# Optimization experiments

Hardware: AMD Instinct MI355X
Metric: run time of the kernel (lower is better)

Reference implementation:

```python
import jax, jax.numpy as jnp
import numpy as np

B, T, C = 2, 2048, 1024
H = 16
HD = C // H  # 64


def setup_inputs() -> dict:
    key = jax.random.key(0)
    ks = jax.random.split(key, 6)
    s_in = 1.0 / np.sqrt(C)
    s_pr = 1.0 / np.sqrt(H * HD)
    x = jax.random.normal(ks[0], (B, T, C), dtype=jnp.float32)
    Wq = jax.random.uniform(ks[1], (H, C, HD), jnp.float32, -s_in, s_in)
    Wk = jax.random.uniform(ks[2], (H, C, HD), jnp.float32, -s_in, s_in)
    Wv = jax.random.uniform(ks[3], (H, C, HD), jnp.float32, -s_in, s_in)
    Wp = jax.random.uniform(ks[4], (H * HD, C), jnp.float32, -s_pr, s_pr)
    bp = jax.random.uniform(ks[5], (C,), jnp.float32, -s_pr, s_pr)
    return {"x": x, "Wq": Wq, "Wk": Wk, "Wv": Wv, "Wp": Wp, "bp": bp}


def reference(x, Wq, Wk, Wv, Wp, bp):
    # per-head projections: [B,T,C] x [H,C,D] -> [B,H,T,D]
    q = jnp.einsum('btc,hcd->bhtd', x, Wq)
    k = jnp.einsum('btc,hcd->bhtd', x, Wk)
    v = jnp.einsum('btc,hcd->bhtd', x, Wv)
    scale = HD ** (-0.5)
    scores = jnp.einsum('bhtd,bhsd->bhts', q, k) * scale  # [B,H,T,T]
    causal = jnp.tril(jnp.ones((T, T), dtype=bool))
    scores = jnp.where(causal, scores, -jnp.inf)
    w = jax.nn.softmax(scores, axis=-1)
    out = jnp.einsum('bhts,bhsd->bhtd', w, v)  # [B,H,T,D]
    # concat heads: [B,T,H*D] (head order matches torch.cat over heads)
    out = jnp.transpose(out, (0, 2, 1, 3)).reshape(B, T, H * HD)
    return out @ Wp + bp
```

## Files before the change

### kernel.cpp

```cpp
#include <hip/hip_runtime.h>
#include <hip/hip_bf16.h>

#define B_NUM 2
#define T_SEQ 2048
#define C_DIM 1024
#define H_NUM 16
#define HD    64
#define M_TOT 4096
#define BH_N  32

typedef __attribute__((ext_vector_type(8))) short short8;
typedef __attribute__((ext_vector_type(4))) float floatx4;

__device__ __forceinline__ short f2bf(float f) {
    unsigned u = __float_as_uint(f);
    u += 0x7FFFu + ((u >> 16) & 1u);
    return (short)(u >> 16);
}

__device__ __forceinline__ unsigned pk2bf(float a, float b) {
    float2 f2; f2.x = a; f2.y = b;
    __hip_bfloat162 h = __float22bfloat162_rn(f2);
    unsigned u; __builtin_memcpy(&u, &h, 4); return u;
}

__device__ __forceinline__ void gld16(const short* g, short* l) {
    __builtin_amdgcn_global_load_lds(
        (const __attribute__((address_space(1))) void*)g,
        (__attribute__((address_space(3))) void*)l, 16, 0, 0);
}

__global__ __launch_bounds__(256) void prep(
    const float* __restrict__ x, const float* __restrict__ Wq,
    const float* __restrict__ Wk, const float* __restrict__ Wv,
    const float* __restrict__ Wp,
    short* __restrict__ xb, short* __restrict__ wt, short* __restrict__ wpt) {
    const int bid = blockIdx.x;
    const int tid = threadIdx.x;
    if (bid < 2048) {
        int idx = (bid * 256 + tid) * 8;
        float4 a = *(const float4*)(x + idx);
        float4 b = *(const float4*)(x + idx + 4);
        short8 o;
        o[0] = f2bf(a.x); o[1] = f2bf(a.y); o[2] = f2bf(a.z); o[3] = f2bf(a.w);
        o[4] = f2bf(b.x); o[5] = f2bf(b.y); o[6] = f2bf(b.z); o[7] = f2bf(b.w);
        *(short8*)(xb + idx) = o;
        return;
    }
    const int b2 = bid - 2048;
    const int ct = b2 & 15, y = b2 >> 4;
    __shared__ short sh[64][72];
    if (y < 48) {
        const int which = y >> 4, h = y & 15;
        const float* W = ((which == 0) ? Wq : (which == 1) ? Wk : Wv) + (size_t)h * C_DIM * HD;
        const int c0 = ct * 64;
        #pragma unroll
        for (int p = 0; p < 4; ++p) {
            int idx = tid + 256 * p;
            int c = idx >> 4, d4 = idx & 15;
            float4 v = *(const float4*)(W + (size_t)(c0 + c) * HD + d4 * 4);
            sh[d4 * 4 + 0][c] = f2bf(v.x);
            sh[d4 * 4 + 1][c] = f2bf(v.y);
            sh[d4 * 4 + 2][c] = f2bf(v.z);
            sh[d4 * 4 + 3][c] = f2bf(v.w);
        }
        __syncthreads();
        #pragma unroll
        for (int p = 0; p < 2; ++p) {
            int idx = tid + 256 * p;
            int d = idx >> 3, cc = idx & 7;
            short8 vv = *(const short8*)(&sh[d][cc * 8]);
            *(short8*)(wt + ((size_t)(which * 16 + h) * 64 + d) * C_DIM + c0 + cc * 8) = vv;
        }
    } else {
        const int nt = y - 48;
        #pragma unroll
        for (int p = 0; p < 4; ++p) {
            int idx = tid + 256 * p;
            int k = idx >> 4, n4 = idx & 15;
            float4 v = *(const float4*)(Wp + (size_t)(ct * 64 + k) * C_DIM + nt * 64 + n4 * 4);
            sh[n4 * 4 + 0][k] = f2bf(v.x);
            sh[n4 * 4 + 1][k] = f2bf(v.y);
            sh[n4 * 4 + 2][k] = f2bf(v.z);
            sh[n4 * 4 + 3][k] = f2bf(v.w);
        }
        __syncthreads();
        #pragma unroll
        for (int p = 0; p < 2; ++p) {
            int idx = tid + 256 * p;
            int n = idx >> 3, cc = idx & 7;
            short8 vv = *(const short8*)(&sh[n][cc * 8]);
            *(short8*)(wpt + (size_t)(nt * 64 + n) * C_DIM + ct * 64 + cc * 8) = vv;
        }
    }
}

__global__ __launch_bounds__(256) void qkv_gemm(
    const short* __restrict__ xb, const short* __restrict__ wt,
    short* __restrict__ qb, short* __restrict__ kb, short* __restrict__ vtb) {
    const int mt = blockIdx.x, ntg = blockIdx.y;
    const int m0 = mt * 128, n0 = ntg * 128;
    const int which = ntg >> 3;
    const float sc = (which == 0) ? 0.125f * 1.4426950408889634f : 1.0f;

    __shared__ short smem[17408];
    short* As = smem;
    short* Bs = smem + 8192;

    const int tid = threadIdx.x;
    const int lane = tid & 63, w = tid >> 6;
    const int wm = w & 1, wn = w >> 1;
    const int hi = lane >> 4, llo = lane & 15;
    const int lrow = lane >> 3;
    const int lswz = ((lane & 7) ^ (lrow & 7)) * 8;
    const int fc0 = (hi ^ (llo & 7)) * 8;
    const int fc1 = ((hi + 4) ^ (llo & 7)) * 8;

    floatx4 acc[4][4];
    #pragma unroll
    for (int i = 0; i < 4; ++i)
        #pragma unroll
        for (int j = 0; j < 4; ++j)
            #pragma unroll
            for (int r = 0; r < 4; ++r) acc[i][j][r] = 0.0f;

    const size_t a_base = (size_t)(m0 + w * 32 + lrow) * C_DIM + lswz;
    const size_t b_base = (size_t)(n0 + w * 32 + lrow) * C_DIM + lswz;

    for (int kt = 0; kt < C_DIM / 64; ++kt) {
        const int c0 = kt * 64;
        __syncthreads();
        #pragma unroll
        for (int p = 0; p < 4; ++p) {
            gld16(xb + a_base + (size_t)p * 8 * C_DIM + c0, &As[(w * 32 + p * 8) * 64]);
            gld16(wt + b_base + (size_t)p * 8 * C_DIM + c0, &Bs[(w * 32 + p * 8) * 64]);
        }
        __syncthreads();

        short8 af[4][2];
        #pragma unroll
        for (int mi = 0; mi < 4; ++mi) {
            const int row = wm * 64 + mi * 16 + llo;
            af[mi][0] = *(const short8*)(&As[row * 64 + fc0]);
            af[mi][1] = *(const short8*)(&As[row * 64 + fc1]);
        }
        #pragma unroll
        for (int ni = 0; ni < 4; ++ni) {
            const int row = wn * 64 + ni * 16 + llo;
            short8 b0 = *(const short8*)(&Bs[row * 64 + fc0]);
            short8 b1 = *(const short8*)(&Bs[row * 64 + fc1]);
            #pragma unroll
            for (int mi = 0; mi < 4; ++mi) {
                acc[mi][ni] = __builtin_amdgcn_mfma_f32_16x16x32_bf16(af[mi][0], b0, acc[mi][ni], 0, 0, 0);
                acc[mi][ni] = __builtin_amdgcn_mfma_f32_16x16x32_bf16(af[mi][1], b1, acc[mi][ni], 0, 0, 0);
            }
        }
    }
    __syncthreads();

    short (*R)[136] = (short(*)[136])smem;
    if (which == 2) {
        #pragma unroll
        for (int mi = 0; mi < 4; ++mi)
            #pragma unroll
            for (int ni = 0; ni < 4; ++ni)
                #pragma unroll
                for (int r = 0; r < 4; ++r)
                    R[wn * 64 + ni * 16 + llo][wm * 64 + mi * 16 + hi * 4 + r] =
                        f2bf(acc[mi][ni][r]);
        __syncthreads();
        const int b = m0 >> 11;
        #pragma unroll
        for (int p = 0; p < 8; ++p) {
            int idx = tid + 256 * p;
            int rr = idx >> 4, cc = idx & 15;
            short8 vv = *(const short8*)(&R[rr][cc * 8]);
            int n = n0 + rr;
            int h = (n >> 6) & 15, d = n & 63;
            int t = (m0 & 2047) + cc * 8;
            *(short8*)(vtb + ((size_t)((b * H_NUM + h) * HD + d)) * T_SEQ + t) = vv;
        }
    } else {
        short* outp = (which == 0) ? qb : kb;
        #pragma unroll
        for (int mi = 0; mi < 4; ++mi)
            #pragma unroll
            for (int ni = 0; ni < 4; ++ni)
                #pragma unroll
                for (int r = 0; r < 4; ++r)
                    R[wm * 64 + mi * 16 + hi * 4 + r][wn * 64 + ni * 16 + llo] =
                        f2bf(acc[mi][ni][r] * sc);
        __syncthreads();
        #pragma unroll
        for (int p = 0; p < 8; ++p) {
            int idx = tid + 256 * p;
            int r = idx >> 4, cc = idx & 15;
            short8 vv = *(const short8*)(&R[r][cc * 8]);
            int mg = m0 + r;
            int b = mg >> 11, t = mg & 2047;
            int n = n0 + cc * 8;
            int h = (n >> 6) & 15, d = n & 63;
            *(short8*)(outp + ((size_t)(b * H_NUM + h) * T_SEQ + t) * HD + d) = vv;
        }
    }
}

__global__ __launch_bounds__(512) void attn_mfma(
    const short* __restrict__ qb, const short* __restrict__ kb,
    const short* __restrict__ vtb, short* __restrict__ attb) {
    const int bh = blockIdx.x;
    const int y = blockIdx.y;
    const int qt = (y < 8) ? (15 - y) : (y - 8);
    const int b = bh >> 4, h = bh & 15;
    const short* K  = kb  + (size_t)bh * T_SEQ * HD;
    const short* Vt = vtb + (size_t)bh * HD * T_SEQ;

    __shared__ short Ks[2][4096];
    __shared__ short Vs[2][4096];
    __shared__ short Ones[16 * 64];
    __shared__ short Ps[128][76];

    const int tid = threadIdx.x;
    const int lane = tid & 63, w = tid >> 6;
    const int hi = lane >> 4, llo = lane & 15;
    const int lrow = lane >> 3;
    const int lswz = ((lane & 7) ^ (lrow & 7)) * 8;
    const int fc0 = (hi ^ (llo & 7)) * 8;
    const int fc1 = ((hi + 4) ^ (llo & 7)) * 8;
    const int kmax = 2 * qt + 1;

    short8 qf[2];
    const int qcol0 = qt * 128 + w * 16;
    #pragma unroll
    for (int kh = 0; kh < 2; ++kh)
        qf[kh] = *(const short8*)(qb +
            ((size_t)bh * T_SEQ + qcol0 + llo) * HD + kh * 32 + hi * 8);

    for (int i = tid; i < 16 * 64; i += 512)
        Ones[i] = (i < 64) ? (short)0x3F80 : (short)0;

    gld16(K + (size_t)(w * 8 + lrow) * HD + lswz, &Ks[0][(w * 8) * 64]);
    gld16(Vt + (size_t)(w * 8 + lrow) * T_SEQ + lswz, &Vs[0][(w * 8) * 64]);

    floatx4 Oa[5];
    #pragma unroll
    for (int n = 0; n < 5; ++n)
        #pragma unroll
        for (int r = 0; r < 4; ++r) Oa[n][r] = 0.0f;

    for (int kt = 0; kt <= kmax; ++kt) {
        __syncthreads();
        const int buf = kt & 1;

        if (kt + 1 <= kmax) {
            const int s0 = (kt + 1) * 64;
            const int nb = buf ^ 1;
            gld16(K + ((size_t)s0 + w * 8 + lrow) * HD + lswz, &Ks[nb][(w * 8) * 64]);
            gld16(Vt + (size_t)(w * 8 + lrow) * T_SEQ + s0 + lswz, &Vs[nb][(w * 8) * 64]);
        }

        short8 ak[4][2];
        #pragma unroll
        for (int nt = 0; nt < 4; ++nt) {
            const int row = nt * 16 + llo;
            ak[nt][0] = *(const short8*)(&Ks[buf][row * 64 + fc0]);
            ak[nt][1] = *(const short8*)(&Ks[buf][row * 64 + fc1]);
        }
        floatx4 sf[4];
        #pragma unroll
        for (int nt = 0; nt < 4; ++nt)
            #pragma unroll
            for (int r = 0; r < 4; ++r) sf[nt][r] = 0.0f;
        #pragma unroll
        for (int nt = 0; nt < 4; ++nt)
            #pragma unroll
            for (int kh = 0; kh < 2; ++kh)
                sf[nt] = __builtin_amdgcn_mfma_f32_16x16x32_bf16(
                    ak[nt][kh], qf[kh], sf[nt], 0, 0, 0);

        const int sbase = kt * 64;
        if (sbase + 63 > qcol0) {
            const int qlane = qcol0 + llo;
            #pragma unroll
            for (int nt = 0; nt < 4; ++nt)
                #pragma unroll
                for (int r = 0; r < 4; ++r)
                    if (sbase + nt * 16 + hi * 4 + r > qlane) sf[nt][r] = -3.0e38f;
        }

        #pragma unroll
        for (int nt = 0; nt < 4; ++nt) {
            float p0 = __builtin_amdgcn_exp2f(sf[nt][0]);
            float p1 = __builtin_amdgcn_exp2f(sf[nt][1]);
            float p2 = __builtin_amdgcn_exp2f(sf[nt][2]);
            float p3 = __builtin_amdgcn_exp2f(sf[nt][3]);
            uint2 u; u.x = pk2bf(p0, p1); u.y = pk2bf(p2, p3);
            *(uint2*)(&Ps[w * 16 + llo][nt * 16 + hi * 4]) = u;
        }

        short8 av[5][2];
        #pragma unroll
        for (int nt2 = 0; nt2 < 4; ++nt2) {
            const int row = nt2 * 16 + llo;
            av[nt2][0] = *(const short8*)(&Vs[buf][row * 64 + fc0]);
            av[nt2][1] = *(const short8*)(&Vs[buf][row * 64 + fc1]);
        }
        av[4][0] = *(const short8*)(&Ones[llo * 64 + fc0]);
        av[4][1] = *(const short8*)(&Ones[llo * 64 + fc1]);
        short8 bp[2];
        #pragma unroll
        for (int kh = 0; kh < 2; ++kh)
            bp[kh] = *(const short8*)(&Ps[w * 16 + llo][kh * 32 + hi * 8]);
        #pragma unroll
        for (int nt2 = 0; nt2 < 5; ++nt2)
            #pragma unroll
            for (int kh = 0; kh < 2; ++kh)
                Oa[nt2] = __builtin_amdgcn_mfma_f32_16x16x32_bf16(
                    av[nt2][kh], bp[kh], Oa[nt2], 0, 0, 0);
    }

    {
        float lb = __shfl(Oa[4][0], llo);
        float inv = 1.0f / lb;
        #pragma unroll
        for (int nt2 = 0; nt2 < 4; ++nt2) {
            uint2 u;
            u.x = pk2bf(Oa[nt2][0] * inv, Oa[nt2][1] * inv);
            u.y = pk2bf(Oa[nt2][2] * inv, Oa[nt2][3] * inv);
            *(uint2*)(&Ps[w * 16 + llo][nt2 * 16 + hi * 4]) = u;
        }
    }
    __syncthreads();
    #pragma unroll
    for (int p = 0; p < 2; ++p) {
        int idx = tid + 512 * p;
        int r = idx >> 3, cc = idx & 7;
        short8 vv = *(const short8*)(&Ps[r][cc * 8]);
        *(short8*)(attb + ((size_t)(b * T_SEQ + qt * 128 + r)) * C_DIM + h * HD + cc * 8) = vv;
    }
}

__global__ __launch_bounds__(256) void proj_gemm(
    const short* __restrict__ attb, const short* __restrict__ wpt,
    const float* __restrict__ bp, float* __restrict__ out) {
    const int mt = blockIdx.x, nt_g = blockIdx.y;
    const int m0 = mt * 128, n0 = nt_g * 64;

    __shared__ short As[8192];
    __shared__ short Bs[4096];

    const int tid = threadIdx.x;
    const int lane = tid & 63, w = tid >> 6;
    const int hi = lane >> 4, llo = lane & 15;
    const int lrow = lane >> 3;
    const int lswz = ((lane & 7) ^ (lrow & 7)) * 8;
    const int fc0 = (hi ^ (llo & 7)) * 8;
    const int fc1 = ((hi + 4) ^ (llo & 7)) * 8;

    floatx4 acc[2][4];
    #pragma unroll
    for (int i = 0; i < 2; ++i)
        #pragma unroll
        for (int j = 0; j < 4; ++j)
            #pragma unroll
            for (int r = 0; r < 4; ++r) acc[i][j][r] = 0.0f;

    const size_t a_base = (size_t)(m0 + w * 32 + lrow) * C_DIM + lswz;
    const size_t b_base = (size_t)(n0 + w * 16 + lrow) * C_DIM + lswz;

    for (int kt = 0; kt < C_DIM / 64; ++kt) {
        const int c0 = kt * 64;
        __syncthreads();
        #pragma unroll
        for (int p = 0; p < 4; ++p)
            gld16(attb + a_base + (size_t)p * 8 * C_DIM + c0, &As[(w * 32 + p * 8) * 64]);
        #pragma unroll
        for (int p = 0; p < 2; ++p)
            gld16(wpt + b_base + (size_t)p * 8 * C_DIM + c0, &Bs[(w * 16 + p * 8) * 64]);
        __syncthreads();

        short8 af[2][2];
        #pragma unroll
        for (int m2 = 0; m2 < 2; ++m2) {
            const int row = w * 32 + m2 * 16 + llo;
            af[m2][0] = *(const short8*)(&As[row * 64 + fc0]);
            af[m2][1] = *(const short8*)(&As[row * 64 + fc1]);
        }
        #pragma unroll
        for (int nt = 0; nt < 4; ++nt) {
            const int row = nt * 16 + llo;
            short8 b0 = *(const short8*)(&Bs[row * 64 + fc0]);
            short8 b1 = *(const short8*)(&Bs[row * 64 + fc1]);
            #pragma unroll
            for (int m2 = 0; m2 < 2; ++m2) {
                acc[m2][nt] = __builtin_amdgcn_mfma_f32_16x16x32_bf16(af[m2][0], b0, acc[m2][nt], 0, 0, 0);
                acc[m2][nt] = __builtin_amdgcn_mfma_f32_16x16x32_bf16(af[m2][1], b1, acc[m2][nt], 0, 0, 0);
            }
        }
    }

    #pragma unroll
    for (int nt = 0; nt < 4; ++nt) {
        const int n = n0 + nt * 16 + llo;
        const float bias = bp[n];
        #pragma unroll
        for (int m2 = 0; m2 < 2; ++m2)
            #pragma unroll
            for (int r = 0; r < 4; ++r) {
                int m = m0 + w * 32 + m2 * 16 + hi * 4 + r;
                out[(size_t)m * C_DIM + n] = acc[m2][nt][r] + bias;
            }
    }
}

extern "C" void kernel_launch(void* const* d_in, const int* in_sizes, int n_in,
                              void* d_out, int out_size, void* d_ws, size_t ws_size,
                              hipStream_t stream) {
    const float* x  = (const float*)d_in[0];
    const float* Wq = (const float*)d_in[1];
    const float* Wk = (const float*)d_in[2];
    const float* Wv = (const float*)d_in[3];
    const float* Wp = (const float*)d_in[4];
    const float* bp = (const float*)d_in[5];
    float* out = (float*)d_out;

    short* xb   = (short*)d_ws;
    short* wt   = xb  + (size_t)M_TOT * C_DIM;
    short* wpt  = wt  + (size_t)3 * H_NUM * HD * C_DIM;
    short* qb   = wpt + (size_t)C_DIM * C_DIM;
    short* kb   = qb  + (size_t)M_TOT * C_DIM;
    short* vtb  = kb  + (size_t)M_TOT * C_DIM;
    short* attb = vtb + (size_t)M_TOT * C_DIM;

    prep     <<<dim3(3072), 256, 0, stream>>>(x, Wq, Wk, Wv, Wp, xb, wt, wpt);
    qkv_gemm <<<dim3(M_TOT / 128, 3 * C_DIM / 128), 256, 0, stream>>>(xb, wt, qb, kb, vtb);
    attn_mfma<<<dim3(BH_N, T_SEQ / 128), 512, 0, stream>>>(qb, kb, vtb, attb);
    proj_gemm<<<dim3(M_TOT / 128, C_DIM / 64), 256, 0, stream>>>(attb, wpt, bp, out);
}
```

Baseline: 179.4 us.

## Fuse all four stages into one cooperative persistent kernel with grid syncs

Replaces the four separate launches (prep, QKV GEMM, attention, projection) with a single persistent cooperative kernel that loops over work units per stage and separates the stages with grid.sync(). The QKV GEMM tile also changes to 128x192 with 512 threads. The goal is to remove launch gaps and tail effects between kernels. The cost is grid-wide barriers, a fixed grid of 256 or 512 blocks that may load-balance worse than the old grids, and added register and LDS pressure from one shared buffer sized for every stage. The original kernels remain as a fallback if the cooperative launch fails.

```diff
diff --git a/kernel.cpp b/kernel.cpp
--- a/kernel.cpp
+++ b/kernel.cpp
@@ -1,5 +1,8 @@
 #include <hip/hip_runtime.h>
 #include <hip/hip_bf16.h>
+#include <hip/hip_cooperative_groups.h>
+
+namespace cg = cooperative_groups;
 
 #define B_NUM 2
 #define T_SEQ 2048
@@ -30,7 +33,376 @@
         (__attribute__((address_space(3))) void*)l, 16, 0, 0);
 }
 
-__global__ __launch_bounds__(256) void prep(
+__global__ __launch_bounds__(512, 4) void mega(
+    const float* __restrict__ x,  const float* __restrict__ Wq,
+    const float* __restrict__ Wk, const float* __restrict__ Wv,
+    const float* __restrict__ Wp, const float* __restrict__ bp,
+    short* __restrict__ xb, short* __restrict__ wt, short* __restrict__ wpt,
+    short* __restrict__ qb, short* __restrict__ kb, short* __restrict__ vtb,
+    short* __restrict__ attb, float* __restrict__ out) {
+
+    __shared__ short smem[26112];
+    cg::grid_group grid = cg::this_grid();
+
+    const int G   = gridDim.x;
+    const int bid = blockIdx.x;
+    const int tid = threadIdx.x;
+    const int lane = tid & 63, w = tid >> 6;
+    const int hi = lane >> 4, llo = lane & 15;
+    const int lrow = lane >> 3;
+    const int lswz = ((lane & 7) ^ (lrow & 7)) * 8;
+    const int fc0 = (hi ^ (llo & 7)) * 8;
+    const int fc1 = ((hi + 4) ^ (llo & 7)) * 8;
+
+    {
+        int gtid = bid * 512 + tid;
+        for (int i = gtid; i < 524288; i += G * 512) {
+            int idx = i * 8;
+            float4 a = *(const float4*)(x + idx);
+            float4 b4 = *(const float4*)(x + idx + 4);
+            short8 o;
+            o[0] = f2bf(a.x);  o[1] = f2bf(a.y);  o[2] = f2bf(a.z);  o[3] = f2bf(a.w);
+            o[4] = f2bf(b4.x); o[5] = f2bf(b4.y); o[6] = f2bf(b4.z); o[7] = f2bf(b4.w);
+            *(short8*)(xb + idx) = o;
+        }
+        short (*sh)[72] = (short(*)[72])smem;
+        for (int unit = bid; unit < 1024; unit += G) {
+            __syncthreads();
+            if (unit < 768) {
+                const int y = unit >> 4, ct = unit & 15;
+                const int which = y >> 4, h = y & 15;
+                const float* W = ((which == 0) ? Wq : (which == 1) ? Wk : Wv)
+                                 + (size_t)h * C_DIM * HD;
+                const int c0 = ct * 64;
+                #pragma unroll
+                for (int p = 0; p < 2; ++p) {
+                    int idx = tid + 512 * p;
+                    int c = idx >> 4, d4 = idx & 15;
+                    float4 v = *(const float4*)(W + (size_t)(c0 + c) * HD + d4 * 4);
+                    sh[d4 * 4 + 0][c] = f2bf(v.x);
+                    sh[d4 * 4 + 1][c] = f2bf(v.y);
+                    sh[d4 * 4 + 2][c] = f2bf(v.z);
+                    sh[d4 * 4 + 3][c] = f2bf(v.w);
+                }
+                __syncthreads();
+                int d = tid >> 3, cc = tid & 7;
+                short8 vv = *(const short8*)(&sh[d][cc * 8]);
+                *(short8*)(wt + ((size_t)(which * 16 + h) * 64 + d) * C_DIM + c0 + cc * 8) = vv;
+            } else {
+                const int u2 = unit - 768;
+                const int nt = u2 >> 4, ct = u2 & 15;
+                #pragma unroll
+                for (int p = 0; p < 2; ++p) {
+                    int idx = tid + 512 * p;
+                    int k = idx >> 4, n4 = idx & 15;
+                    float4 v = *(const float4*)(Wp + (size_t)(ct * 64 + k) * C_DIM + nt * 64 + n4 * 4);
+                    sh[n4 * 4 + 0][k] = f2bf(v.x);
+                    sh[n4 * 4 + 1][k] = f2bf(v.y);
+                    sh[n4 * 4 + 2][k] = f2bf(v.z);
+                    sh[n4 * 4 + 3][k] = f2bf(v.w);
+                }
+                __syncthreads();
+                int n = tid >> 3, cc = tid & 7;
+                short8 vv = *(const short8*)(&sh[n][cc * 8]);
+                *(short8*)(wpt + (size_t)(nt * 64 + n) * C_DIM + ct * 64 + cc * 8) = vv;
+            }
+        }
+    }
+    grid.sync();
+
+    for (int tile = bid; tile < 512; tile += G) {
+        const int mt = tile >> 4, ntg = tile & 15;
+        const int m0 = mt * 128, n0 = ntg * 192;
+        const int wm = w & 1, wn = w >> 1;
+        short* As = smem;
+        short* Bs = smem + 8192;
+
+        floatx4 acc[4][3];
+        #pragma unroll
+        for (int i = 0; i < 4; ++i)
+            #pragma unroll
+            for (int j = 0; j < 3; ++j)
+                #pragma unroll
+                for (int r = 0; r < 4; ++r) acc[i][j][r] = 0.0f;
+
+        const size_t a_base = (size_t)(m0 + w * 16 + lrow) * C_DIM + lswz;
+        const size_t b_base = (size_t)(n0 + w * 24 + lrow) * C_DIM + lswz;
+
+        for (int kt = 0; kt < C_DIM / 64; ++kt) {
+            const int c0 = kt * 64;
+            __syncthreads();
+            #pragma unroll
+            for (int p = 0; p < 2; ++p)
+                gld16(xb + a_base + (size_t)p * 8 * C_DIM + c0, &As[(w * 16 + p * 8) * 64]);
+            #pragma unroll
+            for (int p = 0; p < 3; ++p)
+                gld16(wt + b_base + (size_t)p * 8 * C_DIM + c0, &Bs[(w * 24 + p * 8) * 64]);
+            __syncthreads();
+
+            short8 af[4][2];
+            #pragma unroll
+            for (int mi = 0; mi < 4; ++mi) {
+                const int row = wm * 64 + mi * 16 + llo;
+                af[mi][0] = *(const short8*)(&As[row * 64 + fc0]);
+                af[mi][1] = *(const short8*)(&As[row * 64 + fc1]);
+            }
+            #pragma unroll
+            for (int ni = 0; ni < 3; ++ni) {
+                const int row = wn * 48 + ni * 16 + llo;
+                short8 b0 = *(const short8*)(&Bs[row * 64 + fc0]);
+                short8 b1 = *(const short8*)(&Bs[row * 64 + fc1]);
+                #pragma unroll
+                for (int mi = 0; mi < 4; ++mi) {
+                    acc[mi][ni] = __builtin_amdgcn_mfma_f32_16x16x32_bf16(af[mi][0], b0, acc[mi][ni], 0, 0, 0);
+                    acc[mi][ni] = __builtin_amdgcn_mfma_f32_16x16x32_bf16(af[mi][1], b1, acc[mi][ni], 0, 0, 0);
+                }
+            }
+        }
+
+        const int bb = m0 >> 11;
+        #pragma unroll
+        for (int c = 0; c < 3; ++c) {
+            const int n_chunk = n0 + 64 * c;
+            const int which = n_chunk >> 10;
+            const int h = (n_chunk >> 6) & 15;
+            __syncthreads();
+            if (which == 2) {
+                short (*R)[136] = (short(*)[136])smem;
+                #pragma unroll
+                for (int ni = 0; ni < 3; ++ni) {
+                    const int gcol = wn * 48 + ni * 16;
+                    if ((gcol >> 6) == c) {
+                        #pragma unroll
+                        for (int mi = 0; mi < 4; ++mi)
+                            #pragma unroll
+                            for (int r = 0; r < 4; ++r)
+                                R[(gcol & 63) + llo][wm * 64 + mi * 16 + hi * 4 + r] =
+                                    f2bf(acc[mi][ni][r]);
+                    }
+                }
+                __syncthreads();
+                #pragma unroll
+                for (int p = 0; p < 2; ++p) {
+                    int idx = tid + 512 * p;
+                    int rr = idx >> 4, cc = idx & 15;
+                    short8 vv = *(const short8*)(&R[rr][cc * 8]);
+                    int t = (m0 & 2047) + cc * 8;
+                    *(short8*)(vtb + ((size_t)((bb * H_NUM + h) * HD + rr)) * T_SEQ + t) = vv;
+                }
+            } else {
+                short (*R)[72] = (short(*)[72])smem;
+                const float scl = (which == 0) ? 0.125f * 1.4426950408889634f : 1.0f;
+                #pragma unroll
+                for (int ni = 0; ni < 3; ++ni) {
+                    const int gcol = wn * 48 + ni * 16;
+                    if ((gcol >> 6) == c) {
+                        #pragma unroll
+                        for (int mi = 0; mi < 4; ++mi)
+                            #pragma unroll
+                            for (int r = 0; r < 4; ++r)
+                                R[wm * 64 + mi * 16 + hi * 4 + r][(gcol & 63) + llo] =
+                                    f2bf(acc[mi][ni][r] * scl);
+                    }
+                }
+                __syncthreads();
+                short* outp = (which == 0) ? qb : kb;
+                #pragma unroll
+                for (int p = 0; p < 2; ++p) {
+                    int idx = tid + 512 * p;
+                    int r = idx >> 3, cc = idx & 7;
+                    short8 vv = *(const short8*)(&R[r][cc * 8]);
+                    int t = (m0 + r) & 2047;
+                    *(short8*)(outp + ((size_t)(bb * H_NUM + h) * T_SEQ + t) * HD + cc * 8) = vv;
+                }
+            }
+        }
+    }
+    grid.sync();
+
+    for (int unit = bid; unit < 512; unit += G) {
+        const int bh = unit & 31;
+        const int y = unit >> 5;
+        const int qt = (y < 8) ? (15 - y) : (y - 8);
+        const int b = bh >> 4, h = bh & 15;
+        const short* K  = kb  + (size_t)bh * T_SEQ * HD;
+        const short* Vt = vtb + (size_t)bh * HD * T_SEQ;
+
+        short* Ks = smem;
+        short* Vs = smem + 8192;
+        short (*Ps)[76] = (short(*)[76])(smem + 16384);
+
+        const int kmax = 2 * qt + 1;
+
+        short8 qf[2];
+        const int qcol0 = qt * 128 + w * 16;
+        #pragma unroll
+        for (int kh = 0; kh < 2; ++kh)
+            qf[kh] = *(const short8*)(qb +
+                ((size_t)bh * T_SEQ + qcol0 + llo) * HD + kh * 32 + hi * 8);
+
+        short8 av4;
+        #pragma unroll
+        for (int j = 0; j < 8; ++j) av4[j] = (llo == 0) ? (short)0x3F80 : (short)0;
+
+        gld16(K + (size_t)(w * 8 + lrow) * HD + lswz, &Ks[(w * 8) * 64]);
+        gld16(Vt + (size_t)(w * 8 + lrow) * T_SEQ + lswz, &Vs[(w * 8) * 64]);
+
+        floatx4 Oa[5];
+        #pragma unroll
+        for (int n = 0; n < 5; ++n)
+            #pragma unroll
+            for (int r = 0; r < 4; ++r) Oa[n][r] = 0.0f;
+
+        for (int kt = 0; kt <= kmax; ++kt) {
+            __syncthreads();
+            const int buf = (kt & 1) * 4096;
+
+            if (kt + 1 <= kmax) {
+                const int s0 = (kt + 1) * 64;
+                const int nb = ((kt + 1) & 1) * 4096;
+                gld16(K + ((size_t)s0 + w * 8 + lrow) * HD + lswz, &Ks[nb + (w * 8) * 64]);
+                gld16(Vt + (size_t)(w * 8 + lrow) * T_SEQ + s0 + lswz, &Vs[nb + (w * 8) * 64]);
+            }
+
+            short8 ak[4][2];
+            #pragma unroll
+            for (int nt = 0; nt < 4; ++nt) {
+                const int row = nt * 16 + llo;
+                ak[nt][0] = *(const short8*)(&Ks[buf + row * 64 + fc0]);
+                ak[nt][1] = *(const short8*)(&Ks[buf + row * 64 + fc1]);
+            }
+            floatx4 sf[4];
+            #pragma unroll
+            for (int nt = 0; nt < 4; ++nt)
+                #pragma unroll
+                for (int r = 0; r < 4; ++r) sf[nt][r] = 0.0f;
+            #pragma unroll
+            for (int nt = 0; nt < 4; ++nt)
+                #pragma unroll
+                for (int kh = 0; kh < 2; ++kh)
+                    sf[nt] = __builtin_amdgcn_mfma_f32_16x16x32_bf16(
+                        ak[nt][kh], qf[kh], sf[nt], 0, 0, 0);
+
+            const int sbase = kt * 64;
+            if (sbase + 63 > qcol0) {
+                const int qlane = qcol0 + llo;
+                #pragma unroll
+                for (int nt = 0; nt < 4; ++nt)
+                    #pragma unroll
+                    for (int r = 0; r < 4; ++r)
+                        if (sbase + nt * 16 + hi * 4 + r > qlane) sf[nt][r] = -3.0e38f;
+            }
+
+            #pragma unroll
+            for (int nt = 0; nt < 4; ++nt) {
+                float p0 = __builtin_amdgcn_exp2f(sf[nt][0]);
+                float p1 = __builtin_amdgcn_exp2f(sf[nt][1]);
+                float p2 = __builtin_amdgcn_exp2f(sf[nt][2]);
+                float p3 = __builtin_amdgcn_exp2f(sf[nt][3]);
+                uint2 u; u.x = pk2bf(p0, p1); u.y = pk2bf(p2, p3);
+                *(uint2*)(&Ps[w * 16 + llo][nt * 16 + hi * 4]) = u;
+            }
+
+            short8 av[5][2];
+            #pragma unroll
+            for (int nt2 = 0; nt2 < 4; ++nt2) {
+                const int row = nt2 * 16 + llo;
+                av[nt2][0] = *(const short8*)(&Vs[buf + row * 64 + fc0]);
+                av[nt2][1] = *(const short8*)(&Vs[buf + row * 64 + fc1]);
+            }
+            av[4][0] = av4;
+            av[4][1] = av4;
+            short8 bpf[2];
+            #pragma unroll
+            for (int kh = 0; kh < 2; ++kh)
+                bpf[kh] = *(const short8*)(&Ps[w * 16 + llo][kh * 32 + hi * 8]);
+            #pragma unroll
+            for (int nt2 = 0; nt2 < 5; ++nt2)
+                #pragma unroll
+                for (int kh = 0; kh < 2; ++kh)
+                    Oa[nt2] = __builtin_amdgcn_mfma_f32_16x16x32_bf16(
+                        av[nt2][kh], bpf[kh], Oa[nt2], 0, 0, 0);
+        }
+
+        {
+            float lb = __shfl(Oa[4][0], llo);
+            float inv = 1.0f / lb;
+            #pragma unroll
+            for (int nt2 = 0; nt2 < 4; ++nt2) {
+                uint2 u;
+                u.x = pk2bf(Oa[nt2][0] * inv, Oa[nt2][1] * inv);
+                u.y = pk2bf(Oa[nt2][2] * inv, Oa[nt2][3] * inv);
+                *(uint2*)(&Ps[w * 16 + llo][nt2 * 16 + hi * 4]) = u;
+            }
+        }
+        __syncthreads();
+        #pragma unroll
+        for (int p = 0; p < 2; ++p) {
+            int idx = tid + 512 * p;
+            int r = idx >> 3, cc = idx & 7;
+            short8 vv = *(const short8*)(&Ps[r][cc * 8]);
+            *(short8*)(attb + ((size_t)(b * T_SEQ + qt * 128 + r)) * C_DIM + h * HD + cc * 8) = vv;
+        }
+        __syncthreads();
+    }
+    grid.sync();
+
+    for (int tile = bid; tile < 512; tile += G) {
+        const int mt = tile >> 4, ntg = tile & 15;
+        const int m0 = mt * 128, n0 = ntg * 64;
+        const int wm = w & 1, wn = w >> 1;
+        short* As = smem;
+        short* Bs = smem + 8192;
+
+        floatx4 acc[4];
+        #pragma unroll
+        for (int i = 0; i < 4; ++i)
+            #pragma unroll
+            for (int r = 0; r < 4; ++r) acc[i][r] = 0.0f;
+
+        const size_t a_base = (size_t)(m0 + w * 16 + lrow) * C_DIM + lswz;
+        const size_t b_base = (size_t)(n0 + w * 8 + lrow) * C_DIM + lswz;
+
+        for (int kt = 0; kt < C_DIM / 64; ++kt) {
+            const int c0 = kt * 64;
+            __syncthreads();
+            #pragma unroll
+            for (int p = 0; p < 2; ++p)
+                gld16(attb + a_base + (size_t)p * 8 * C_DIM + c0, &As[(w * 16 + p * 8) * 64]);
+            gld16(wpt + b_base + c0, &Bs[(w * 8) * 64]);
+            __syncthreads();
+
+            short8 af[4][2];
+            #pragma unroll
+            for (int mi = 0; mi < 4; ++mi) {
+                const int row = wm * 64 + mi * 16 + llo;
+                af[mi][0] = *(const short8*)(&As[row * 64 + fc0]);
+                af[mi][1] = *(const short8*)(&As[row * 64 + fc1]);
+            }
+            const int brow = wn * 16 + llo;
+            short8 b0 = *(const short8*)(&Bs[brow * 64 + fc0]);
+            short8 b1 = *(const short8*)(&Bs[brow * 64 + fc1]);
+            #pragma unroll
+            for (int mi = 0; mi < 4; ++mi) {
+                acc[mi] = __builtin_amdgcn_mfma_f32_16x16x32_bf16(af[mi][0], b0, acc[mi], 0, 0, 0);
+                acc[mi] = __builtin_amdgcn_mfma_f32_16x16x32_bf16(af[mi][1], b1, acc[mi], 0, 0, 0);
+            }
+        }
+
+        const int n = n0 + wn * 16 + llo;
+        const float bias = bp[n];
+        #pragma unroll
+        for (int mi = 0; mi < 4; ++mi)
+            #pragma unroll
+            for (int r = 0; r < 4; ++r) {
+                int m = m0 + wm * 64 + mi * 16 + hi * 4 + r;
+                out[(size_t)m * C_DIM + n] = acc[mi][r] + bias;
+            }
+        __syncthreads();
+    }
+}
+
+__global__ __launch_bounds__(256) void prep_k(
     const float* __restrict__ x, const float* __restrict__ Wq,
     const float* __restrict__ Wk, const float* __restrict__ Wv,
     const float* __restrict__ Wp,
@@ -95,7 +467,7 @@
     }
 }
 
-__global__ __launch_bounds__(256) void qkv_gemm(
+__global__ __launch_bounds__(256) void qkv_k(
     const short* __restrict__ xb, const short* __restrict__ wt,
     short* __restrict__ qb, short* __restrict__ kb, short* __restrict__ vtb) {
     const int mt = blockIdx.x, ntg = blockIdx.y;
@@ -205,7 +577,7 @@
     }
 }
 
-__global__ __launch_bounds__(512) void attn_mfma(
+__global__ __launch_bounds__(512) void attn_k(
     const short* __restrict__ qb, const short* __restrict__ kb,
     const short* __restrict__ vtb, short* __restrict__ attb) {
     const int bh = blockIdx.x;
@@ -307,16 +679,16 @@
         }
         av[4][0] = *(const short8*)(&Ones[llo * 64 + fc0]);
         av[4][1] = *(const short8*)(&Ones[llo * 64 + fc1]);
-        short8 bp[2];
+        short8 bpf[2];
         #pragma unroll
         for (int kh = 0; kh < 2; ++kh)
-            bp[kh] = *(const short8*)(&Ps[w * 16 + llo][kh * 32 + hi * 8]);
+            bpf[kh] = *(const short8*)(&Ps[w * 16 + llo][kh * 32 + hi * 8]);
         #pragma unroll
         for (int nt2 = 0; nt2 < 5; ++nt2)
             #pragma unroll
             for (int kh = 0; kh < 2; ++kh)
                 Oa[nt2] = __builtin_amdgcn_mfma_f32_16x16x32_bf16(
-                    av[nt2][kh], bp[kh], Oa[nt2], 0, 0, 0);
+                    av[nt2][kh], bpf[kh], Oa[nt2], 0, 0, 0);
     }
 
     {
@@ -340,7 +712,7 @@
     }
 }
 
-__global__ __launch_bounds__(256) void proj_gemm(
+__global__ __launch_bounds__(256) void proj_k(
     const short* __restrict__ attb, const short* __restrict__ wpt,
     const float* __restrict__ bp, float* __restrict__ out) {
     const int mt = blockIdx.x, nt_g = blockIdx.y;
@@ -432,8 +804,25 @@
     short* vtb  = kb  + (size_t)M_TOT * C_DIM;
     short* attb = vtb + (size_t)M_TOT * C_DIM;
 
-    prep     <<<dim3(3072), 256, 0, stream>>>(x, Wq, Wk, Wv, Wp, xb, wt, wpt);
-    qkv_gemm <<<dim3(M_TOT / 128, 3 * C_DIM / 128), 256, 0, stream>>>(xb, wt, qb, kb, vtb);
-    attn_mfma<<<dim3(BH_N, T_SEQ / 128), 512, 0, stream>>>(qb, kb, vtb, attb);
-    proj_gemm<<<dim3(M_TOT / 128, C_DIM / 64), 256, 0, stream>>>(attb, wpt, bp, out);
+    int maxBlk = 0;
+    hipError_t qe = hipOccupancyMaxActiveBlocksPerMultiprocessor(&maxBlk, mega, 512, 0);
+    int gridN = 256;
+    if (qe == hipSuccess && maxBlk >= 2) gridN = 512;
+
+    void* args[] = { (void*)&x, (void*)&Wq, (void*)&Wk, (void*)&Wv,
+                     (void*)&Wp, (void*)&bp,
+                     (void*)&xb, (void*)&wt, (void*)&wpt,
+                     (void*)&qb, (void*)&kb, (void*)&vtb, (void*)&attb,
+                     (void*)&out };
+    hipError_t le = hipErrorUnknown;
+    if (qe == hipSuccess && maxBlk >= 1)
+        le = hipLaunchCooperativeKernel((void*)mega, dim3(gridN), dim3(512),
+                                        args, 0, stream);
+    if (le != hipSuccess) {
+        (void)hipGetLastError();
+        prep_k<<<dim3(3072), 256, 0, stream>>>(x, Wq, Wk, Wv, Wp, xb, wt, wpt);
+        qkv_k <<<dim3(M_TOT / 128, 3 * C_DIM / 128), 256, 0, stream>>>(xb, wt, qb, kb, vtb);
+        attn_k<<<dim3(BH_N, T_SEQ / 128), 512, 0, stream>>>(qb, kb, vtb, attb);
+        proj_k<<<dim3(M_TOT / 128, C_DIM / 64), 256, 0, stream>>>(attb, wpt, bp, out);
+    }
 }
```

Measured after the change: 312.2 us. +74.0%, slower.

## Switch attention to 32x32x16 MFMA with 4 waves and register row-sum

Applied to the files above, without the earlier changes.

The attention kernel moves from 8 waves using 16x16x32 MFMAs to 4 waves (256 threads, launch bounds 256,2) using 32x32x16 MFMAs, so each wave handles 32 query rows. The softmax denominator is now accumulated in registers from the exponentials and combined with a cross-lane shuffle. This replaces the extra MFMA against an LDS 'Ones' matrix and drops that buffer. The larger MFMA shape gives more compute per LDS fragment load, at the cost of fewer waves per block and more accumulator registers. The row sum is taken from fp32 probabilities while the P·V product uses bf16-rounded values, a small numeric inconsistency.

```diff
diff --git a/kernel.cpp b/kernel.cpp
--- a/kernel.cpp
+++ b/kernel.cpp
@@ -11,6 +11,7 @@
 
 typedef __attribute__((ext_vector_type(8))) short short8;
 typedef __attribute__((ext_vector_type(4))) float floatx4;
+typedef __attribute__((ext_vector_type(16))) float floatx16;
 
 __device__ __forceinline__ short f2bf(float f) {
     unsigned u = __float_as_uint(f);
@@ -30,7 +31,7 @@
         (__attribute__((address_space(3))) void*)l, 16, 0, 0);
 }
 
-__global__ __launch_bounds__(256) void prep(
+__global__ __launch_bounds__(256) void prep_k(
     const float* __restrict__ x, const float* __restrict__ Wq,
     const float* __restrict__ Wk, const float* __restrict__ Wv,
     const float* __restrict__ Wp,
@@ -95,7 +96,7 @@
     }
 }
 
-__global__ __launch_bounds__(256) void qkv_gemm(
+__global__ __launch_bounds__(256) void qkv_k(
     const short* __restrict__ xb, const short* __restrict__ wt,
     short* __restrict__ qb, short* __restrict__ kb, short* __restrict__ vtb) {
     const int mt = blockIdx.x, ntg = blockIdx.y;
@@ -205,7 +206,7 @@
     }
 }
 
-__global__ __launch_bounds__(512) void attn_mfma(
+__global__ __launch_bounds__(256, 2) void attn_k(
     const short* __restrict__ qb, const short* __restrict__ kb,
     const short* __restrict__ vtb, short* __restrict__ attb) {
     const int bh = blockIdx.x;
@@ -217,36 +218,36 @@
 
     __shared__ short Ks[2][4096];
     __shared__ short Vs[2][4096];
-    __shared__ short Ones[16 * 64];
     __shared__ short Ps[128][76];
 
     const int tid = threadIdx.x;
     const int lane = tid & 63, w = tid >> 6;
-    const int hi = lane >> 4, llo = lane & 15;
+    const int nq = lane & 31, kh2 = lane >> 5;
     const int lrow = lane >> 3;
     const int lswz = ((lane & 7) ^ (lrow & 7)) * 8;
-    const int fc0 = (hi ^ (llo & 7)) * 8;
-    const int fc1 = ((hi + 4) ^ (llo & 7)) * 8;
     const int kmax = 2 * qt + 1;
-
-    short8 qf[2];
-    const int qcol0 = qt * 128 + w * 16;
-    #pragma unroll
-    for (int kh = 0; kh < 2; ++kh)
-        qf[kh] = *(const short8*)(qb +
-            ((size_t)bh * T_SEQ + qcol0 + llo) * HD + kh * 32 + hi * 8);
-
-    for (int i = tid; i < 16 * 64; i += 512)
-        Ones[i] = (i < 64) ? (short)0x3F80 : (short)0;
-
-    gld16(K + (size_t)(w * 8 + lrow) * HD + lswz, &Ks[0][(w * 8) * 64]);
-    gld16(Vt + (size_t)(w * 8 + lrow) * T_SEQ + lswz, &Vs[0][(w * 8) * 64]);
-
-    floatx4 Oa[5];
-    #pragma unroll
-    for (int n = 0; n < 5; ++n)
-        #pragma unroll
-        for (int r = 0; r < 4; ++r) Oa[n][r] = 0.0f;
+    const int qcol0 = qt * 128 + w * 32;
+
+    short8 qf[4];
+    #pragma unroll
+    for (int t = 0; t < 4; ++t)
+        qf[t] = *(const short8*)(qb +
+            ((size_t)bh * T_SEQ + qcol0 + nq) * HD + t * 16 + kh2 * 8);
+
+    #pragma unroll
+    for (int p = 0; p < 2; ++p) {
+        gld16(K + (size_t)(w * 16 + p * 8 + lrow) * HD + lswz,
+              &Ks[0][(w * 16 + p * 8) * 64]);
+        gld16(Vt + (size_t)(w * 16 + p * 8 + lrow) * T_SEQ + lswz,
+              &Vs[0][(w * 16 + p * 8) * 64]);
+    }
+
+    floatx16 Oa[2];
+    #pragma unroll
+    for (int dt = 0; dt < 2; ++dt)
+        #pragma unroll
+        for (int r = 0; r < 16; ++r) Oa[dt][r] = 0.0f;
+    float l_acc = 0.0f;
 
     for (int kt = 0; kt <= kmax; ++kt) {
         __syncthreads();
@@ -255,92 +256,93 @@
         if (kt + 1 <= kmax) {
             const int s0 = (kt + 1) * 64;
             const int nb = buf ^ 1;
-            gld16(K + ((size_t)s0 + w * 8 + lrow) * HD + lswz, &Ks[nb][(w * 8) * 64]);
-            gld16(Vt + (size_t)(w * 8 + lrow) * T_SEQ + s0 + lswz, &Vs[nb][(w * 8) * 64]);
-        }
-
-        short8 ak[4][2];
-        #pragma unroll
-        for (int nt = 0; nt < 4; ++nt) {
-            const int row = nt * 16 + llo;
-            ak[nt][0] = *(const short8*)(&Ks[buf][row * 64 + fc0]);
-            ak[nt][1] = *(const short8*)(&Ks[buf][row * 64 + fc1]);
-        }
-        floatx4 sf[4];
-        #pragma unroll
-        for (int nt = 0; nt < 4; ++nt)
-            #pragma unroll
-            for (int r = 0; r < 4; ++r) sf[nt][r] = 0.0f;
-        #pragma unroll
-        for (int nt = 0; nt < 4; ++nt)
-            #pragma unroll
-            for (int kh = 0; kh < 2; ++kh)
-                sf[nt] = __builtin_amdgcn_mfma_f32_16x16x32_bf16(
-                    ak[nt][kh], qf[kh], sf[nt], 0, 0, 0);
+            #pragma unroll
+            for (int p = 0; p < 2; ++p) {
+                gld16(K + ((size_t)s0 + w * 16 + p * 8 + lrow) * HD + lswz,
+                      &Ks[nb][(w * 16 + p * 8) * 64]);
+                gld16(Vt + (size_t)(w * 16 + p * 8 + lrow) * T_SEQ + s0 + lswz,
+                      &Vs[nb][(w * 16 + p * 8) * 64]);
+            }
+        }
+
+        floatx16 sf[2];
+        #pragma unroll
+        for (int st = 0; st < 2; ++st)
+            #pragma unroll
+            for (int r = 0; r < 16; ++r) sf[st][r] = 0.0f;
+        #pragma unroll
+        for (int t = 0; t < 4; ++t)
+            #pragma unroll
+            for (int st = 0; st < 2; ++st) {
+                const int row = st * 32 + nq;
+                short8 a = *(const short8*)(
+                    &Ks[buf][row * 64 + (((t * 2 + kh2) ^ (row & 7)) * 8)]);
+                sf[st] = __builtin_amdgcn_mfma_f32_32x32x16_bf16(
+                    a, qf[t], sf[st], 0, 0, 0);
+            }
 
         const int sbase = kt * 64;
         if (sbase + 63 > qcol0) {
-            const int qlane = qcol0 + llo;
-            #pragma unroll
-            for (int nt = 0; nt < 4; ++nt)
+            const int qg = qcol0 + nq;
+            #pragma unroll
+            for (int st = 0; st < 2; ++st)
                 #pragma unroll
-                for (int r = 0; r < 4; ++r)
-                    if (sbase + nt * 16 + hi * 4 + r > qlane) sf[nt][r] = -3.0e38f;
-        }
-
-        #pragma unroll
-        for (int nt = 0; nt < 4; ++nt) {
-            float p0 = __builtin_amdgcn_exp2f(sf[nt][0]);
-            float p1 = __builtin_amdgcn_exp2f(sf[nt][1]);
-            float p2 = __builtin_amdgcn_exp2f(sf[nt][2]);
-            float p3 = __builtin_amdgcn_exp2f(sf[nt][3]);
-            uint2 u; u.x = pk2bf(p0, p1); u.y = pk2bf(p2, p3);
-            *(uint2*)(&Ps[w * 16 + llo][nt * 16 + hi * 4]) = u;
-        }
-
-        short8 av[5][2];
-        #pragma unroll
-        for (int nt2 = 0; nt2 < 4; ++nt2) {
-            const int row = nt2 * 16 + llo;
-            av[nt2][0] = *(const short8*)(&Vs[buf][row * 64 + fc0]);
-            av[nt2][1] = *(const short8*)(&Vs[buf][row * 64 + fc1]);
-        }
-        av[4][0] = *(const short8*)(&Ones[llo * 64 + fc0]);
-        av[4][1] = *(const short8*)(&Ones[llo * 64 + fc1]);
-        short8 bp[2];
-        #pragma unroll
-        for (int kh = 0; kh < 2; ++kh)
-            bp[kh] = *(const short8*)(&Ps[w * 16 + llo][kh * 32 + hi * 8]);
-        #pragma unroll
-        for (int nt2 = 0; nt2 < 5; ++nt2)
-            #pragma unroll
-            for (int kh = 0; kh < 2; ++kh)
-                Oa[nt2] = __builtin_amdgcn_mfma_f32_16x16x32_bf16(
-                    av[nt2][kh], bp[kh], Oa[nt2], 0, 0, 0);
-    }
-
-    {
-        float lb = __shfl(Oa[4][0], llo);
-        float inv = 1.0f / lb;
-        #pragma unroll
-        for (int nt2 = 0; nt2 < 4; ++nt2) {
+                for (int r = 0; r < 16; ++r) {
+                    int m = (r & 3) + 8 * (r >> 2) + 4 * kh2;
+                    if (sbase + st * 32 + m > qg) sf[st][r] = -3.0e38f;
+                }
+        }
+
+        #pragma unroll
+        for (int st = 0; st < 2; ++st)
+            #pragma unroll
+            for (int g = 0; g < 4; ++g) {
+                float p0 = __builtin_amdgcn_exp2f(sf[st][4 * g + 0]);
+                float p1 = __builtin_amdgcn_exp2f(sf[st][4 * g + 1]);
+                float p2 = __builtin_amdgcn_exp2f(sf[st][4 * g + 2]);
+                float p3 = __builtin_amdgcn_exp2f(sf[st][4 * g + 3]);
+                l_acc += (p0 + p1) + (p2 + p3);
+                uint2 u; u.x = pk2bf(p0, p1); u.y = pk2bf(p2, p3);
+                *(uint2*)(&Ps[w * 32 + nq][st * 32 + 8 * g + 4 * kh2]) = u;
+            }
+
+        #pragma unroll
+        for (int t = 0; t < 4; ++t) {
+            short8 bpf = *(const short8*)(&Ps[w * 32 + nq][t * 16 + kh2 * 8]);
+            #pragma unroll
+            for (int dt = 0; dt < 2; ++dt) {
+                const int row = dt * 32 + nq;
+                short8 a = *(const short8*)(
+                    &Vs[buf][row * 64 + (((t * 2 + kh2) ^ (row & 7)) * 8)]);
+                Oa[dt] = __builtin_amdgcn_mfma_f32_32x32x16_bf16(
+                    a, bpf, Oa[dt], 0, 0, 0);
+            }
+        }
+    }
+
+    float l_full = l_acc + __shfl_xor(l_acc, 32);
+    float inv = 1.0f / l_full;
+
+    #pragma unroll
+    for (int dt = 0; dt < 2; ++dt)
+        #pragma unroll
+        for (int g = 0; g < 4; ++g) {
             uint2 u;
-            u.x = pk2bf(Oa[nt2][0] * inv, Oa[nt2][1] * inv);
-            u.y = pk2bf(Oa[nt2][2] * inv, Oa[nt2][3] * inv);
-            *(uint2*)(&Ps[w * 16 + llo][nt2 * 16 + hi * 4]) = u;
-        }
-    }
+            u.x = pk2bf(Oa[dt][4 * g + 0] * inv, Oa[dt][4 * g + 1] * inv);
+            u.y = pk2bf(Oa[dt][4 * g + 2] * inv, Oa[dt][4 * g + 3] * inv);
+            *(uint2*)(&Ps[w * 32 + nq][dt * 32 + 8 * g + 4 * kh2]) = u;
+        }
     __syncthreads();
     #pragma unroll
-    for (int p = 0; p < 2; ++p) {
-        int idx = tid + 512 * p;
+    for (int p = 0; p < 4; ++p) {
+        int idx = tid + 256 * p;
         int r = idx >> 3, cc = idx & 7;
         short8 vv = *(const short8*)(&Ps[r][cc * 8]);
         *(short8*)(attb + ((size_t)(b * T_SEQ + qt * 128 + r)) * C_DIM + h * HD + cc * 8) = vv;
     }
 }
 
-__global__ __launch_bounds__(256) void proj_gemm(
+__global__ __launch_bounds__(256) void proj_k(
     const short* __restrict__ attb, const short* __restrict__ wpt,
     const float* __restrict__ bp, float* __restrict__ out) {
     const int mt = blockIdx.x, nt_g = blockIdx.y;
@@ -432,8 +434,8 @@
     short* vtb  = kb  + (size_t)M_TOT * C_DIM;
     short* attb = vtb + (size_t)M_TOT * C_DIM;
 
-    prep     <<<dim3(3072), 256, 0, stream>>>(x, Wq, Wk, Wv, Wp, xb, wt, wpt);
-    qkv_gemm <<<dim3(M_TOT / 128, 3 * C_DIM / 128), 256, 0, stream>>>(xb, wt, qb, kb, vtb);
-    attn_mfma<<<dim3(BH_N, T_SEQ / 128), 512, 0, stream>>>(qb, kb, vtb, attb);
-    proj_gemm<<<dim3(M_TOT / 128, C_DIM / 64), 256, 0, stream>>>(attb, wpt, bp, out);
-}
+    prep_k<<<dim3(3072), 256, 0, stream>>>(x, Wq, Wk, Wv, Wp, xb, wt, wpt);
+    qkv_k <<<dim3(M_TOT / 128, 3 * C_DIM / 128), 256, 0, stream>>>(xb, wt, qb, kb, vtb);
+    attn_k<<<dim3(BH_N, T_SEQ / 128), 256, 0, stream>>>(qb, kb, vtb, attb);
+    proj_k<<<dim3(M_TOT / 128, C_DIM / 64), 256, 0, stream>>>(attb, wpt, bp, out);
+}
```

Result: no change. 182.7 us (+1.8%).
